# Kernel tuning notes

Measured on AMD Instinct MI355X. Metric: run time of the kernel, lower is better.

The kernel has to match this reference:

```python
import jax, jax.numpy as jnp
import numpy as np

D_MODEL = 512
N_HEADS = 8
D_K = D_MODEL // N_HEADS
WINDOW = 64
SCALE = 1.0 / np.sqrt(D_K)


def setup_inputs() -> dict:
    key = jax.random.key(0)
    ks = jax.random.split(key, 9)
    B, S = 1, 2048
    s = 1.0 / np.sqrt(D_MODEL)
    inp = {
        "x": jax.random.normal(ks[0], (B, S, D_MODEL), dtype=jnp.float32),
        "Wq": jax.random.normal(ks[1], (D_MODEL, D_MODEL), dtype=jnp.float32) * s,
        "bq": jnp.zeros((D_MODEL,), dtype=jnp.float32),
        "Wk": jax.random.normal(ks[2], (D_MODEL, D_MODEL), dtype=jnp.float32) * s,
        "bk": jnp.zeros((D_MODEL,), dtype=jnp.float32),
        "Wv": jax.random.normal(ks[3], (D_MODEL, D_MODEL), dtype=jnp.float32) * s,
        "bv": jnp.zeros((D_MODEL,), dtype=jnp.float32),
        "Wo": jax.random.normal(ks[4], (D_MODEL, D_MODEL), dtype=jnp.float32) * s,
        "bo": jnp.zeros((D_MODEL,), dtype=jnp.float32),
    }
    return inp


def reference(x, Wq, bq, Wk, bk, Wv, bv, Wo, bo):
    B, S, _ = x.shape
    # projections (torch Linear: x @ W.T + b); split heads -> [B,S,H,dk]
    q = (x @ Wq.T + bq).reshape(B, S, N_HEADS, D_K)
    k = (x @ Wk.T + bk).reshape(B, S, N_HEADS, D_K)
    v = (x @ Wv.T + bv).reshape(B, S, N_HEADS, D_K)

    # banded window indices: position i attends to [i-W, i+W]
    L = 2 * WINDOW + 1
    offsets = jnp.arange(L) - WINDOW                    # [L]
    pos = jnp.arange(S)[:, None] + offsets[None, :]     # [S, L]
    valid = (pos >= 0) & (pos < S)                      # [S, L]
    posc = jnp.clip(pos, 0, S - 1)

    k_w = k[:, posc]                                    # [B, S, L, H, dk]
    v_w = v[:, posc]                                    # [B, S, L, H, dk]

    scores = jnp.einsum("bshd,bslhd->bhsl", q, k_w) * SCALE
    scores = jnp.where(valid[None, None, :, :], scores, -jnp.inf)
    attn = jax.nn.softmax(scores, axis=-1)              # [B, H, S, L]
    out = jnp.einsum("bhsl,bslhd->bshd", attn, v_w)     # [B, S, H, dk]
    out = out.reshape(B, S, D_MODEL)
    return out @ Wo.T + bo
```

## Files before the change

### kernel.cpp

```cpp
#include <hip/hip_runtime.h>
#include <hip/hip_bf16.h>
#include <math.h>

#define S_LEN  2048
#define DMODEL 512
#define NHEADS 8
#define DK     64
#define WIN    64

static constexpr float SCALE = 0.125f;

typedef short bf16x8 __attribute__((ext_vector_type(8)));
typedef float f32x4  __attribute__((ext_vector_type(4)));

__device__ __forceinline__ short bfh(float v)
{
    __hip_bfloat16 b = __float2bfloat16(v);
    return *reinterpret_cast<short*>(&b);
}
__device__ __forceinline__ float bf2f(short s)
{
    __hip_bfloat16 b = *reinterpret_cast<__hip_bfloat16*>(&s);
    return __bfloat162float(b);
}
__device__ __forceinline__ void split1(float v, short& h, short& l)
{
    h = bfh(v);
    l = bfh(v - bf2f(h));
}

__device__ __forceinline__ void dma16(const void* g, void* l)
{
    __builtin_amdgcn_global_load_lds(
        (const __attribute__((address_space(1))) unsigned int*)g,
        (__attribute__((address_space(3))) unsigned int*)l, 16, 0, 0);
}

__global__ __launch_bounds__(256)
void prep(const float* __restrict__ x,
          const float* __restrict__ wq, const float* __restrict__ wk,
          const float* __restrict__ wv, const float* __restrict__ wo,
          short* __restrict__ xh, short* __restrict__ xl,
          short* __restrict__ wqb, short* __restrict__ wkb,
          short* __restrict__ wvb, short* __restrict__ wob)
{
    const int z = blockIdx.z;
    if (z == 0) {
        for (int i = blockIdx.x * 256 + threadIdx.x; i < 262144; i += gridDim.x * 256) {
            const float4 v = ((const float4*)x)[i];
            short4 h4, l4;
            split1(v.x, h4.x, l4.x);
            split1(v.y, h4.y, l4.y);
            split1(v.z, h4.z, l4.z);
            split1(v.w, h4.w, l4.w);
            ((short4*)xh)[i] = h4;
            ((short4*)xl)[i] = l4;
        }
    } else {
        const float* s; short* d;
        switch (z) {
            case 1:  s = wq; d = wqb; break;
            case 2:  s = wk; d = wkb; break;
            case 3:  s = wv; d = wvb; break;
            default: s = wo; d = wob; break;
        }
        for (int i = blockIdx.x * 256 + threadIdx.x; i < 65536; i += gridDim.x * 256) {
            const float4 v = ((const float4*)s)[i];
            short4 o;
            o.x = bfh(v.x); o.y = bfh(v.y); o.z = bfh(v.z); o.w = bfh(v.w);
            ((short4*)d)[i] = o;
        }
    }
}

__global__ __launch_bounds__(256)
void gemm_qkv8(const short* __restrict__ xh, const short* __restrict__ xl,
               const short* __restrict__ wqb, const short* __restrict__ wkb,
               const short* __restrict__ wvb,
               const float* __restrict__ bq, const float* __restrict__ bk,
               const float* __restrict__ bv,
               short* __restrict__ qb, short* __restrict__ kb,
               short* __restrict__ vbt)
{
    __shared__ __align__(16) short sW[64 * 512];

    const int z = blockIdx.z;
    const short* Bg   = (z == 0) ? wqb : (z == 1) ? wkb : wvb;
    const float* bias = (z == 0) ? bq  : (z == 1) ? bk  : bv;
    const int row0 = blockIdx.y * 64;
    const int col0 = blockIdx.x * 64;
    const int tid  = threadIdx.x;
    const int lane = tid & 63;
    const int wv   = tid >> 6;
    const int col  = lane & 15;
    const int quad = lane >> 4;
    const int m    = row0 + wv * 16 + col;

    for (int i = wv; i < 64; i += 4) {
        dma16(Bg + (size_t)(col0 + i) * 512 + (size_t)((lane ^ (i & 7)) * 8),
              sW + i * 512);
    }
    __syncthreads();

    f32x4 acc[4];
#pragma unroll
    for (int nj = 0; nj < 4; ++nj)
        acc[nj] = (f32x4)0.0f;

#pragma unroll 4
    for (int kc = 0; kc < 16; ++kc) {
        const size_t aoff = (size_t)m * 512 + kc * 32 + quad * 8;
        const bf16x8 ah = *(const bf16x8*)(xh + aoff);
        const bf16x8 al = *(const bf16x8*)(xl + aoff);
#pragma unroll
        for (int nj = 0; nj < 4; ++nj) {
            const int n = nj * 16 + col;
            const int c = kc * 4 + quad;
            const bf16x8 bf = *(const bf16x8*)&sW[n * 512 + ((c ^ (n & 7)) * 8)];
            acc[nj] = __builtin_amdgcn_mfma_f32_16x16x32_bf16(ah, bf, acc[nj], 0, 0, 0);
            acc[nj] = __builtin_amdgcn_mfma_f32_16x16x32_bf16(al, bf, acc[nj], 0, 0, 0);
        }
    }

#pragma unroll
    for (int nj = 0; nj < 4; ++nj) {
        const int cc = col0 + nj * 16 + col;
        const float bias_v = bias[cc];
#pragma unroll
        for (int e = 0; e < 4; ++e) {
            const int row = row0 + wv * 16 + quad * 4 + e;
            const float val = acc[nj][e] + bias_v;
            if (z == 0) {
                qb[(size_t)row * 512 + cc] = bfh(val);
            } else if (z == 1) {
                kb[(size_t)row * 512 + cc] = bfh(val);
            } else {
                vbt[(size_t)cc * 2048 + row] = bfh(val);
            }
        }
    }
}

__global__ __launch_bounds__(256)
void gemm_out8(const short* __restrict__ ah_g,
               const short* __restrict__ wob, const float* __restrict__ bo,
               float* __restrict__ out)
{
    __shared__ __align__(16) short sW[64 * 512];

    const int row0 = blockIdx.y * 64;
    const int col0 = blockIdx.x * 64;
    const int tid  = threadIdx.x;
    const int lane = tid & 63;
    const int wv   = tid >> 6;
    const int col  = lane & 15;
    const int quad = lane >> 4;
    const int m    = row0 + wv * 16 + col;

    for (int i = wv; i < 64; i += 4) {
        dma16(wob + (size_t)(col0 + i) * 512 + (size_t)((lane ^ (i & 7)) * 8),
              sW + i * 512);
    }
    __syncthreads();

    f32x4 acc[4];
#pragma unroll
    for (int nj = 0; nj < 4; ++nj)
        acc[nj] = (f32x4)0.0f;

#pragma unroll 4
    for (int kc = 0; kc < 16; ++kc) {
        const bf16x8 af = *(const bf16x8*)(ah_g + (size_t)m * 512 + kc * 32 + quad * 8);
#pragma unroll
        for (int nj = 0; nj < 4; ++nj) {
            const int n = nj * 16 + col;
            const int c = kc * 4 + quad;
            const bf16x8 bf = *(const bf16x8*)&sW[n * 512 + ((c ^ (n & 7)) * 8)];
            acc[nj] = __builtin_amdgcn_mfma_f32_16x16x32_bf16(af, bf, acc[nj], 0, 0, 0);
        }
    }

#pragma unroll
    for (int nj = 0; nj < 4; ++nj) {
        const int cc = col0 + nj * 16 + col;
        const float bias_v = bo[cc];
#pragma unroll
        for (int e = 0; e < 4; ++e) {
            const int row = row0 + wv * 16 + quad * 4 + e;
            out[(size_t)row * 512 + cc] = acc[nj][e] + bias_v;
        }
    }
}

__global__ __launch_bounds__(256)
void banded_attn6(const short* __restrict__ qb, const short* __restrict__ kb,
                  const short* __restrict__ vbt, short* __restrict__ abh)
{
    __shared__ __align__(16) short VtS[64 * 256];
    __shared__ __align__(16) short KS [192 * 64];
    __shared__ __align__(16) short QS [32 * 64];
    __shared__ float pmax[4][32];
    __shared__ float psum[4][32];
    short* PS = KS;

    const int h    = blockIdx.x;
    const int t0   = blockIdx.y * 32;
    const int tid  = threadIdx.x;
    const int lane = tid & 63;
    const int wv   = tid >> 6;
    const int col  = lane & 15;
    const int quad = lane >> 4;

    {
        const int lr = lane >> 3;
        const int lc = lane & 7;
        for (int i = wv; i < 28; i += 4) {
            const short* src; short* dst; int r;
            if (i < 4) {
                r = i * 8 + lr;
                src = qb + (size_t)(t0 + r) * 512 + h * 64;
                dst = QS + i * 512;
            } else {
                const int g = i - 4;
                r = g * 8 + lr;
                int pos = t0 - 64 + r;
                pos = pos < 0 ? 0 : (pos > 2047 ? 2047 : pos);
                src = kb + (size_t)pos * 512 + h * 64;
                dst = KS + g * 512;
            }
            const int cs = lc ^ (r & 7);
            dma16(src + cs * 8, dst);
        }
        for (int i = wv; i < 32; i += 4) {
            const int q = i * 64 + lane;
            const int d = q >> 5;
            const int b = q & 31;
            const int j0 = (b < 24) ? b : 0;
            const int j = j0 ^ (d & 7);
            int p0 = t0 - 64 + j * 8;
            p0 = p0 < 0 ? 0 : (p0 > 2040 ? 2040 : p0);
            dma16(vbt + (size_t)(h * 64 + d) * 2048 + p0, VtS + i * 512);
        }
    }
    __syncthreads();

    f32x4 sacc[2][3];
#pragma unroll
    for (int mi = 0; mi < 2; ++mi)
#pragma unroll
        for (int nj = 0; nj < 3; ++nj)
            sacc[mi][nj] = (f32x4)0.0f;

#pragma unroll
    for (int ks = 0; ks < 2; ++ks) {
        const int q0 = ks * 4 + quad;
        bf16x8 aq[2];
#pragma unroll
        for (int mi = 0; mi < 2; ++mi) {
            const int mm = mi * 16 + col;
            const int p = q0 ^ (mm & 7);
            aq[mi] = *(const bf16x8*)&QS[mm * 64 + p * 8];
        }
#pragma unroll
        for (int nj = 0; nj < 3; ++nj) {
            const int n = wv * 48 + nj * 16 + col;
            const int p = q0 ^ (n & 7);
            const bf16x8 bkf = *(const bf16x8*)&KS[n * 64 + p * 8];
#pragma unroll
            for (int mi = 0; mi < 2; ++mi)
                sacc[mi][nj] = __builtin_amdgcn_mfma_f32_16x16x32_bf16(aq[mi], bkf, sacc[mi][nj], 0, 0, 0);
        }
    }

    float pv[2][3][4];
#pragma unroll
    for (int mi = 0; mi < 2; ++mi)
#pragma unroll
        for (int nj = 0; nj < 3; ++nj)
#pragma unroll
            for (int e = 0; e < 4; ++e) {
                const int r32 = mi * 16 + quad * 4 + e;
                const int n   = wv * 48 + nj * 16 + col;
                const int pos = t0 - 64 + n;
                const int d   = n - r32;
                const bool valid = (pos >= 0) && (pos < S_LEN) && (d >= 0) && (d <= 128);
                pv[mi][nj][e] = valid ? sacc[mi][nj][e] * SCALE : -__builtin_inff();
            }

#pragma unroll
    for (int mi = 0; mi < 2; ++mi)
#pragma unroll
        for (int e = 0; e < 4; ++e) {
            float mx = fmaxf(fmaxf(pv[mi][0][e], pv[mi][1][e]), pv[mi][2][e]);
#pragma unroll
            for (int off = 1; off < 16; off <<= 1)
                mx = fmaxf(mx, __shfl_xor(mx, off));
            if ((lane & 15) == 0) pmax[wv][mi * 16 + quad * 4 + e] = mx;
        }
    __syncthreads();

#pragma unroll
    for (int mi = 0; mi < 2; ++mi)
#pragma unroll
        for (int e = 0; e < 4; ++e) {
            const int r32 = mi * 16 + quad * 4 + e;
            const float m = fmaxf(fmaxf(pmax[0][r32], pmax[1][r32]),
                                  fmaxf(pmax[2][r32], pmax[3][r32]));
            float ss = 0.f;
#pragma unroll
            for (int nj = 0; nj < 3; ++nj) {
                const float p = __expf(pv[mi][nj][e] - m);
                pv[mi][nj][e] = p;
                ss += p;
            }
#pragma unroll
            for (int off = 1; off < 16; off <<= 1)
                ss += __shfl_xor(ss, off);
            if ((lane & 15) == 0) psum[wv][r32] = ss;
#pragma unroll
            for (int nj = 0; nj < 3; ++nj) {
                const int n = wv * 48 + nj * 16 + col;
                PS[r32 * 200 + n] = bfh(pv[mi][nj][e]);
            }
        }
    __syncthreads();

    const int mi = wv >> 1;
    f32x4 oacc[2];
    oacc[0] = (f32x4)0.0f;
    oacc[1] = (f32x4)0.0f;
#pragma unroll
    for (int ks = 0; ks < 6; ++ks) {
        const bf16x8 pa = *(const bf16x8*)&PS[(mi * 16 + col) * 200 + ks * 32 + quad * 8];
#pragma unroll
        for (int t = 0; t < 2; ++t) {
            const int d = ((wv & 1) * 2 + t) * 16 + col;
            const int j = (ks * 4 + quad) ^ (d & 7);
            const bf16x8 vf = *(const bf16x8*)&VtS[d * 256 + j * 8];
            oacc[t] = __builtin_amdgcn_mfma_f32_16x16x32_bf16(pa, vf, oacc[t], 0, 0, 0);
        }
    }

    float linv[4];
#pragma unroll
    for (int e = 0; e < 4; ++e) {
        const int r32 = mi * 16 + quad * 4 + e;
        linv[e] = 1.0f / (psum[0][r32] + psum[1][r32] + psum[2][r32] + psum[3][r32]);
    }
#pragma unroll
    for (int t = 0; t < 2; ++t) {
        const int nj = (wv & 1) * 2 + t;
#pragma unroll
        for (int e = 0; e < 4; ++e) {
            const int r32 = mi * 16 + quad * 4 + e;
            const float val = oacc[t][e] * linv[e];
            const size_t idx = (size_t)(t0 + r32) * 512 + h * 64 + nj * 16 + col;
            abh[idx] = bfh(val);
        }
    }
}

extern "C" void kernel_launch(void* const* d_in, const int* in_sizes, int n_in,
                              void* d_out, int out_size, void* d_ws, size_t ws_size,
                              hipStream_t stream)
{
    const float* x  = (const float*)d_in[0];
    const float* Wq = (const float*)d_in[1];
    const float* bq = (const float*)d_in[2];
    const float* Wk = (const float*)d_in[3];
    const float* bk = (const float*)d_in[4];
    const float* Wv = (const float*)d_in[5];
    const float* bv = (const float*)d_in[6];
    const float* Wo = (const float*)d_in[7];
    const float* bo = (const float*)d_in[8];
    float* out = (float*)d_out;

    char* ws = (char*)d_ws;
    short* qb  = (short*)(ws);
    short* kb  = (short*)(ws + (2u << 20));
    short* vbt = (short*)(ws + (4u << 20));
    short* abh = (short*)(ws + (6u << 20));
    short* xh  = (short*)(ws + (8u << 20));
    short* xl  = (short*)(ws + (10u << 20));
    short* wqb = (short*)(ws + (12u << 20));
    short* wkb = (short*)(ws + (12u << 20) + 1 * (512u << 10));
    short* wvb = (short*)(ws + (12u << 20) + 2 * (512u << 10));
    short* wob = (short*)(ws + (12u << 20) + 3 * (512u << 10));

    dim3 gp(128, 1, 5);
    prep<<<gp, 256, 0, stream>>>(x, Wq, Wk, Wv, Wo,
                                 xh, xl, wqb, wkb, wvb, wob);

    dim3 gq(DMODEL / 64, S_LEN / 64, 3);
    gemm_qkv8<<<gq, 256, 0, stream>>>(xh, xl, wqb, wkb, wvb,
                                      bq, bk, bv, qb, kb, vbt);

    dim3 ga(NHEADS, S_LEN / 32);
    banded_attn6<<<ga, 256, 0, stream>>>(qb, kb, vbt, abh);

    dim3 go(DMODEL / 64, S_LEN / 64);
    gemm_out8<<<go, 256, 0, stream>>>(abh, wob, bo, out);
}
```

Before: 115.6 us.

## Fuse all stages into one cooperative persistent kernel with grid syncs

Replaces the four separate launches (prep, QKV GEMM, banded attention, output GEMM) with a single cooperative kernel of 512 blocks that runs each stage in turn, separated by grid-wide barriers. GEMM tiles shrink to 64x32 so every block does the same share of work, and each block loops over Q, K and V in sequence. The aim is to remove per-launch overhead and the gaps between kernels. In exchange it adds grid.sync costs, lowers per-stage parallelism because each block does serial work, and requires all 512 blocks to be resident at once, two per CU.

```diff
diff --git a/kernel.cpp b/kernel.cpp
--- a/kernel.cpp
+++ b/kernel.cpp
@@ -1,6 +1,9 @@
 #include <hip/hip_runtime.h>
+#include <hip/hip_cooperative_groups.h>
 #include <hip/hip_bf16.h>
 #include <math.h>
+
+namespace cg = cooperative_groups;
 
 #define S_LEN  2048
 #define DMODEL 512
@@ -36,326 +39,300 @@
         (__attribute__((address_space(3))) unsigned int*)l, 16, 0, 0);
 }
 
-__global__ __launch_bounds__(256)
-void prep(const float* __restrict__ x,
-          const float* __restrict__ wq, const float* __restrict__ wk,
-          const float* __restrict__ wv, const float* __restrict__ wo,
-          short* __restrict__ xh, short* __restrict__ xl,
-          short* __restrict__ wqb, short* __restrict__ wkb,
-          short* __restrict__ wvb, short* __restrict__ wob)
-{
-    const int z = blockIdx.z;
-    if (z == 0) {
-        for (int i = blockIdx.x * 256 + threadIdx.x; i < 262144; i += gridDim.x * 256) {
-            const float4 v = ((const float4*)x)[i];
+struct KParams {
+    const float *x, *Wq, *bq, *Wk, *bk, *Wv, *bv, *Wo, *bo;
+    float* out;
+    short *qb, *kb, *vbt, *abh, *xh, *xl, *wqb, *wkb, *wvb, *wob;
+};
+
+__global__ __launch_bounds__(256, 2)
+void fused(KParams p)
+{
+    __shared__ __align__(16) char smem[62464];
+    cg::grid_group grid = cg::this_grid();
+
+    const int bid  = blockIdx.x;
+    const int tid  = threadIdx.x;
+    const int lane = tid & 63;
+    const int wv   = tid >> 6;
+    const int col  = lane & 15;
+    const int quad = lane >> 4;
+
+    {
+        for (int i = bid * 256 + tid; i < 262144; i += 131072) {
+            const float4 v = ((const float4*)p.x)[i];
             short4 h4, l4;
             split1(v.x, h4.x, l4.x);
             split1(v.y, h4.y, l4.y);
             split1(v.z, h4.z, l4.z);
             split1(v.w, h4.w, l4.w);
-            ((short4*)xh)[i] = h4;
-            ((short4*)xl)[i] = l4;
-        }
-    } else {
-        const float* s; short* d;
-        switch (z) {
-            case 1:  s = wq; d = wqb; break;
-            case 2:  s = wk; d = wkb; break;
-            case 3:  s = wv; d = wvb; break;
-            default: s = wo; d = wob; break;
-        }
-        for (int i = blockIdx.x * 256 + threadIdx.x; i < 65536; i += gridDim.x * 256) {
+            ((short4*)p.xh)[i] = h4;
+            ((short4*)p.xl)[i] = l4;
+        }
+        for (int u = bid * 256 + tid; u < 262144; u += 131072) {
+            const int w = u >> 16;
+            const int i = u & 65535;
+            const float* s = (w == 0) ? p.Wq : (w == 1) ? p.Wk : (w == 2) ? p.Wv : p.Wo;
+            short*       d = (w == 0) ? p.wqb : (w == 1) ? p.wkb : (w == 2) ? p.wvb : p.wob;
             const float4 v = ((const float4*)s)[i];
             short4 o;
             o.x = bfh(v.x); o.y = bfh(v.y); o.z = bfh(v.z); o.w = bfh(v.w);
             ((short4*)d)[i] = o;
         }
     }
-}
-
-__global__ __launch_bounds__(256)
-void gemm_qkv8(const short* __restrict__ xh, const short* __restrict__ xl,
-               const short* __restrict__ wqb, const short* __restrict__ wkb,
-               const short* __restrict__ wvb,
-               const float* __restrict__ bq, const float* __restrict__ bk,
-               const float* __restrict__ bv,
-               short* __restrict__ qb, short* __restrict__ kb,
-               short* __restrict__ vbt)
-{
-    __shared__ __align__(16) short sW[64 * 512];
-
-    const int z = blockIdx.z;
-    const short* Bg   = (z == 0) ? wqb : (z == 1) ? wkb : wvb;
-    const float* bias = (z == 0) ? bq  : (z == 1) ? bk  : bv;
-    const int row0 = blockIdx.y * 64;
-    const int col0 = blockIdx.x * 64;
-    const int tid  = threadIdx.x;
-    const int lane = tid & 63;
-    const int wv   = tid >> 6;
-    const int col  = lane & 15;
-    const int quad = lane >> 4;
-    const int m    = row0 + wv * 16 + col;
-
-    for (int i = wv; i < 64; i += 4) {
-        dma16(Bg + (size_t)(col0 + i) * 512 + (size_t)((lane ^ (i & 7)) * 8),
-              sW + i * 512);
+    grid.sync();
+
+    {
+        short* sW = (short*)smem;
+        const int ct   = bid & 15;
+        const int rt   = bid >> 4;
+        const int col0 = ct * 32;
+        const int m    = rt * 64 + wv * 16 + col;
+
+        for (int z = 0; z < 3; ++z) {
+            const short* Bg   = (z == 0) ? p.wqb : (z == 1) ? p.wkb : p.wvb;
+            const float* bias = (z == 0) ? p.bq  : (z == 1) ? p.bk  : p.bv;
+
+            __syncthreads();
+            for (int i = wv; i < 32; i += 4)
+                dma16(Bg + (size_t)(col0 + i) * 512 + (size_t)((lane ^ (i & 7)) * 8),
+                      sW + i * 512);
+            __syncthreads();
+
+            f32x4 acc[2];
+            acc[0] = (f32x4)0.0f;
+            acc[1] = (f32x4)0.0f;
+
+#pragma unroll 4
+            for (int kc = 0; kc < 16; ++kc) {
+                const size_t aoff = (size_t)m * 512 + kc * 32 + quad * 8;
+                const bf16x8 ah = *(const bf16x8*)(p.xh + aoff);
+                const bf16x8 al = *(const bf16x8*)(p.xl + aoff);
+#pragma unroll
+                for (int nj = 0; nj < 2; ++nj) {
+                    const int n = nj * 16 + col;
+                    const int c = kc * 4 + quad;
+                    const bf16x8 bf = *(const bf16x8*)&sW[n * 512 + ((c ^ (n & 7)) * 8)];
+                    acc[nj] = __builtin_amdgcn_mfma_f32_16x16x32_bf16(ah, bf, acc[nj], 0, 0, 0);
+                    acc[nj] = __builtin_amdgcn_mfma_f32_16x16x32_bf16(al, bf, acc[nj], 0, 0, 0);
+                }
+            }
+
+#pragma unroll
+            for (int nj = 0; nj < 2; ++nj) {
+                const int cc = col0 + nj * 16 + col;
+                const float bias_v = bias[cc];
+#pragma unroll
+                for (int e = 0; e < 4; ++e) {
+                    const int row = rt * 64 + wv * 16 + quad * 4 + e;
+                    const float val = acc[nj][e] + bias_v;
+                    if (z == 0)      p.qb[(size_t)row * 512 + cc] = bfh(val);
+                    else if (z == 1) p.kb[(size_t)row * 512 + cc] = bfh(val);
+                    else             p.vbt[(size_t)cc * 2048 + row] = bfh(val);
+                }
+            }
+        }
     }
-    __syncthreads();
-
-    f32x4 acc[4];
-#pragma unroll
-    for (int nj = 0; nj < 4; ++nj)
-        acc[nj] = (f32x4)0.0f;
-
-#pragma unroll 4
-    for (int kc = 0; kc < 16; ++kc) {
-        const size_t aoff = (size_t)m * 512 + kc * 32 + quad * 8;
-        const bf16x8 ah = *(const bf16x8*)(xh + aoff);
-        const bf16x8 al = *(const bf16x8*)(xl + aoff);
-#pragma unroll
-        for (int nj = 0; nj < 4; ++nj) {
-            const int n = nj * 16 + col;
-            const int c = kc * 4 + quad;
-            const bf16x8 bf = *(const bf16x8*)&sW[n * 512 + ((c ^ (n & 7)) * 8)];
-            acc[nj] = __builtin_amdgcn_mfma_f32_16x16x32_bf16(ah, bf, acc[nj], 0, 0, 0);
-            acc[nj] = __builtin_amdgcn_mfma_f32_16x16x32_bf16(al, bf, acc[nj], 0, 0, 0);
-        }
-    }
-
-#pragma unroll
-    for (int nj = 0; nj < 4; ++nj) {
-        const int cc = col0 + nj * 16 + col;
-        const float bias_v = bias[cc];
-#pragma unroll
-        for (int e = 0; e < 4; ++e) {
-            const int row = row0 + wv * 16 + quad * 4 + e;
-            const float val = acc[nj][e] + bias_v;
-            if (z == 0) {
-                qb[(size_t)row * 512 + cc] = bfh(val);
-            } else if (z == 1) {
-                kb[(size_t)row * 512 + cc] = bfh(val);
-            } else {
-                vbt[(size_t)cc * 2048 + row] = bfh(val);
-            }
-        }
-    }
-}
-
-__global__ __launch_bounds__(256)
-void gemm_out8(const short* __restrict__ ah_g,
-               const short* __restrict__ wob, const float* __restrict__ bo,
-               float* __restrict__ out)
-{
-    __shared__ __align__(16) short sW[64 * 512];
-
-    const int row0 = blockIdx.y * 64;
-    const int col0 = blockIdx.x * 64;
-    const int tid  = threadIdx.x;
-    const int lane = tid & 63;
-    const int wv   = tid >> 6;
-    const int col  = lane & 15;
-    const int quad = lane >> 4;
-    const int m    = row0 + wv * 16 + col;
-
-    for (int i = wv; i < 64; i += 4) {
-        dma16(wob + (size_t)(col0 + i) * 512 + (size_t)((lane ^ (i & 7)) * 8),
-              sW + i * 512);
-    }
-    __syncthreads();
-
-    f32x4 acc[4];
-#pragma unroll
-    for (int nj = 0; nj < 4; ++nj)
-        acc[nj] = (f32x4)0.0f;
-
-#pragma unroll 4
-    for (int kc = 0; kc < 16; ++kc) {
-        const bf16x8 af = *(const bf16x8*)(ah_g + (size_t)m * 512 + kc * 32 + quad * 8);
-#pragma unroll
-        for (int nj = 0; nj < 4; ++nj) {
-            const int n = nj * 16 + col;
-            const int c = kc * 4 + quad;
-            const bf16x8 bf = *(const bf16x8*)&sW[n * 512 + ((c ^ (n & 7)) * 8)];
-            acc[nj] = __builtin_amdgcn_mfma_f32_16x16x32_bf16(af, bf, acc[nj], 0, 0, 0);
-        }
-    }
-
-#pragma unroll
-    for (int nj = 0; nj < 4; ++nj) {
-        const int cc = col0 + nj * 16 + col;
-        const float bias_v = bo[cc];
-#pragma unroll
-        for (int e = 0; e < 4; ++e) {
-            const int row = row0 + wv * 16 + quad * 4 + e;
-            out[(size_t)row * 512 + cc] = acc[nj][e] + bias_v;
-        }
-    }
-}
-
-__global__ __launch_bounds__(256)
-void banded_attn6(const short* __restrict__ qb, const short* __restrict__ kb,
-                  const short* __restrict__ vbt, short* __restrict__ abh)
-{
-    __shared__ __align__(16) short VtS[64 * 256];
-    __shared__ __align__(16) short KS [192 * 64];
-    __shared__ __align__(16) short QS [32 * 64];
-    __shared__ float pmax[4][32];
-    __shared__ float psum[4][32];
-    short* PS = KS;
-
-    const int h    = blockIdx.x;
-    const int t0   = blockIdx.y * 32;
-    const int tid  = threadIdx.x;
-    const int lane = tid & 63;
-    const int wv   = tid >> 6;
-    const int col  = lane & 15;
-    const int quad = lane >> 4;
+    grid.sync();
 
     {
-        const int lr = lane >> 3;
-        const int lc = lane & 7;
-        for (int i = wv; i < 28; i += 4) {
-            const short* src; short* dst; int r;
-            if (i < 4) {
-                r = i * 8 + lr;
-                src = qb + (size_t)(t0 + r) * 512 + h * 64;
-                dst = QS + i * 512;
-            } else {
-                const int g = i - 4;
-                r = g * 8 + lr;
-                int pos = t0 - 64 + r;
-                pos = pos < 0 ? 0 : (pos > 2047 ? 2047 : pos);
-                src = kb + (size_t)pos * 512 + h * 64;
-                dst = KS + g * 512;
-            }
-            const int cs = lc ^ (r & 7);
-            dma16(src + cs * 8, dst);
-        }
-        for (int i = wv; i < 32; i += 4) {
-            const int q = i * 64 + lane;
-            const int d = q >> 5;
-            const int b = q & 31;
-            const int j0 = (b < 24) ? b : 0;
-            const int j = j0 ^ (d & 7);
-            int p0 = t0 - 64 + j * 8;
-            p0 = p0 < 0 ? 0 : (p0 > 2040 ? 2040 : p0);
-            dma16(vbt + (size_t)(h * 64 + d) * 2048 + p0, VtS + i * 512);
-        }
-    }
-    __syncthreads();
-
-    f32x4 sacc[2][3];
-#pragma unroll
-    for (int mi = 0; mi < 2; ++mi)
-#pragma unroll
-        for (int nj = 0; nj < 3; ++nj)
-            sacc[mi][nj] = (f32x4)0.0f;
-
-#pragma unroll
-    for (int ks = 0; ks < 2; ++ks) {
-        const int q0 = ks * 4 + quad;
-        bf16x8 aq[2];
-#pragma unroll
-        for (int mi = 0; mi < 2; ++mi) {
-            const int mm = mi * 16 + col;
-            const int p = q0 ^ (mm & 7);
-            aq[mi] = *(const bf16x8*)&QS[mm * 64 + p * 8];
-        }
-#pragma unroll
-        for (int nj = 0; nj < 3; ++nj) {
-            const int n = wv * 48 + nj * 16 + col;
-            const int p = q0 ^ (n & 7);
-            const bf16x8 bkf = *(const bf16x8*)&KS[n * 64 + p * 8];
-#pragma unroll
-            for (int mi = 0; mi < 2; ++mi)
-                sacc[mi][nj] = __builtin_amdgcn_mfma_f32_16x16x32_bf16(aq[mi], bkf, sacc[mi][nj], 0, 0, 0);
-        }
-    }
-
-    float pv[2][3][4];
-#pragma unroll
-    for (int mi = 0; mi < 2; ++mi)
-#pragma unroll
-        for (int nj = 0; nj < 3; ++nj)
+        short* VtS = (short*)smem;
+        short* KS  = (short*)(smem + 32768);
+        short* QS  = (short*)(smem + 57344);
+        float (*pmax)[32] = (float(*)[32])(smem + 61440);
+        float (*psum)[32] = (float(*)[32])(smem + 61952);
+        short* PS = KS;
+
+        const int h  = bid >> 6;
+        const int t0 = (bid & 63) * 32;
+
+        {
+            const int lr = lane >> 3;
+            const int lc = lane & 7;
+            for (int i = wv; i < 28; i += 4) {
+                const short* src; short* dst; int r;
+                if (i < 4) {
+                    r = i * 8 + lr;
+                    src = p.qb + (size_t)(t0 + r) * 512 + h * 64;
+                    dst = QS + i * 512;
+                } else {
+                    const int g = i - 4;
+                    r = g * 8 + lr;
+                    int pos = t0 - 64 + r;
+                    pos = pos < 0 ? 0 : (pos > 2047 ? 2047 : pos);
+                    src = p.kb + (size_t)pos * 512 + h * 64;
+                    dst = KS + g * 512;
+                }
+                const int cs = lc ^ (r & 7);
+                dma16(src + cs * 8, dst);
+            }
+            for (int i = wv; i < 32; i += 4) {
+                const int q = i * 64 + lane;
+                const int d = q >> 5;
+                const int b = q & 31;
+                const int j0 = (b < 24) ? b : 0;
+                const int j = j0 ^ (d & 7);
+                int p0 = t0 - 64 + j * 8;
+                p0 = p0 < 0 ? 0 : (p0 > 2040 ? 2040 : p0);
+                dma16(p.vbt + (size_t)(h * 64 + d) * 2048 + p0, VtS + i * 512);
+            }
+        }
+        __syncthreads();
+
+        f32x4 sacc[2][3];
+#pragma unroll
+        for (int mi = 0; mi < 2; ++mi)
+#pragma unroll
+            for (int nj = 0; nj < 3; ++nj)
+                sacc[mi][nj] = (f32x4)0.0f;
+
+#pragma unroll
+        for (int ks = 0; ks < 2; ++ks) {
+            const int q0 = ks * 4 + quad;
+            bf16x8 aq[2];
+#pragma unroll
+            for (int mi = 0; mi < 2; ++mi) {
+                const int mm = mi * 16 + col;
+                const int pp = q0 ^ (mm & 7);
+                aq[mi] = *(const bf16x8*)&QS[mm * 64 + pp * 8];
+            }
+#pragma unroll
+            for (int nj = 0; nj < 3; ++nj) {
+                const int n = wv * 48 + nj * 16 + col;
+                const int pp = q0 ^ (n & 7);
+                const bf16x8 bkf = *(const bf16x8*)&KS[n * 64 + pp * 8];
+#pragma unroll
+                for (int mi = 0; mi < 2; ++mi)
+                    sacc[mi][nj] = __builtin_amdgcn_mfma_f32_16x16x32_bf16(aq[mi], bkf, sacc[mi][nj], 0, 0, 0);
+            }
+        }
+
+        float pv[2][3][4];
+#pragma unroll
+        for (int mi = 0; mi < 2; ++mi)
+#pragma unroll
+            for (int nj = 0; nj < 3; ++nj)
+#pragma unroll
+                for (int e = 0; e < 4; ++e) {
+                    const int r32 = mi * 16 + quad * 4 + e;
+                    const int n   = wv * 48 + nj * 16 + col;
+                    const int pos = t0 - 64 + n;
+                    const int d   = n - r32;
+                    const bool valid = (pos >= 0) && (pos < S_LEN) && (d >= 0) && (d <= 128);
+                    pv[mi][nj][e] = valid ? sacc[mi][nj][e] * SCALE : -__builtin_inff();
+                }
+
+#pragma unroll
+        for (int mi = 0; mi < 2; ++mi)
+#pragma unroll
+            for (int e = 0; e < 4; ++e) {
+                float mx = fmaxf(fmaxf(pv[mi][0][e], pv[mi][1][e]), pv[mi][2][e]);
+#pragma unroll
+                for (int off = 1; off < 16; off <<= 1)
+                    mx = fmaxf(mx, __shfl_xor(mx, off));
+                if ((lane & 15) == 0) pmax[wv][mi * 16 + quad * 4 + e] = mx;
+            }
+        __syncthreads();
+
+#pragma unroll
+        for (int mi = 0; mi < 2; ++mi)
 #pragma unroll
             for (int e = 0; e < 4; ++e) {
                 const int r32 = mi * 16 + quad * 4 + e;
-                const int n   = wv * 48 + nj * 16 + col;
-                const int pos = t0 - 64 + n;
-                const int d   = n - r32;
-                const bool valid = (pos >= 0) && (pos < S_LEN) && (d >= 0) && (d <= 128);
-                pv[mi][nj][e] = valid ? sacc[mi][nj][e] * SCALE : -__builtin_inff();
-            }
-
-#pragma unroll
-    for (int mi = 0; mi < 2; ++mi)
-#pragma unroll
-        for (int e = 0; e < 4; ++e) {
-            float mx = fmaxf(fmaxf(pv[mi][0][e], pv[mi][1][e]), pv[mi][2][e]);
-#pragma unroll
-            for (int off = 1; off < 16; off <<= 1)
-                mx = fmaxf(mx, __shfl_xor(mx, off));
-            if ((lane & 15) == 0) pmax[wv][mi * 16 + quad * 4 + e] = mx;
-        }
-    __syncthreads();
-
-#pragma unroll
-    for (int mi = 0; mi < 2; ++mi)
+                const float m = fmaxf(fmaxf(pmax[0][r32], pmax[1][r32]),
+                                      fmaxf(pmax[2][r32], pmax[3][r32]));
+                float ss = 0.f;
+#pragma unroll
+                for (int nj = 0; nj < 3; ++nj) {
+                    const float pe = __expf(pv[mi][nj][e] - m);
+                    pv[mi][nj][e] = pe;
+                    ss += pe;
+                }
+#pragma unroll
+                for (int off = 1; off < 16; off <<= 1)
+                    ss += __shfl_xor(ss, off);
+                if ((lane & 15) == 0) psum[wv][r32] = ss;
+#pragma unroll
+                for (int nj = 0; nj < 3; ++nj) {
+                    const int n = wv * 48 + nj * 16 + col;
+                    PS[r32 * 200 + n] = bfh(pv[mi][nj][e]);
+                }
+            }
+        __syncthreads();
+
+        const int mi = wv >> 1;
+        f32x4 oacc[2];
+        oacc[0] = (f32x4)0.0f;
+        oacc[1] = (f32x4)0.0f;
+#pragma unroll
+        for (int ks = 0; ks < 6; ++ks) {
+            const bf16x8 pa = *(const bf16x8*)&PS[(mi * 16 + col) * 200 + ks * 32 + quad * 8];
+#pragma unroll
+            for (int t = 0; t < 2; ++t) {
+                const int d = ((wv & 1) * 2 + t) * 16 + col;
+                const int j = (ks * 4 + quad) ^ (d & 7);
+                const bf16x8 vf = *(const bf16x8*)&VtS[d * 256 + j * 8];
+                oacc[t] = __builtin_amdgcn_mfma_f32_16x16x32_bf16(pa, vf, oacc[t], 0, 0, 0);
+            }
+        }
+
+        float linv[4];
 #pragma unroll
         for (int e = 0; e < 4; ++e) {
             const int r32 = mi * 16 + quad * 4 + e;
-            const float m = fmaxf(fmaxf(pmax[0][r32], pmax[1][r32]),
-                                  fmaxf(pmax[2][r32], pmax[3][r32]));
-            float ss = 0.f;
-#pragma unroll
-            for (int nj = 0; nj < 3; ++nj) {
-                const float p = __expf(pv[mi][nj][e] - m);
-                pv[mi][nj][e] = p;
-                ss += p;
-            }
-#pragma unroll
-            for (int off = 1; off < 16; off <<= 1)
-                ss += __shfl_xor(ss, off);
-            if ((lane & 15) == 0) psum[wv][r32] = ss;
-#pragma unroll
-            for (int nj = 0; nj < 3; ++nj) {
-                const int n = wv * 48 + nj * 16 + col;
-                PS[r32 * 200 + n] = bfh(pv[mi][nj][e]);
-            }
-        }
-    __syncthreads();
-
-    const int mi = wv >> 1;
-    f32x4 oacc[2];
-    oacc[0] = (f32x4)0.0f;
-    oacc[1] = (f32x4)0.0f;
-#pragma unroll
-    for (int ks = 0; ks < 6; ++ks) {
-        const bf16x8 pa = *(const bf16x8*)&PS[(mi * 16 + col) * 200 + ks * 32 + quad * 8];
+            linv[e] = 1.0f / (psum[0][r32] + psum[1][r32] + psum[2][r32] + psum[3][r32]);
+        }
 #pragma unroll
         for (int t = 0; t < 2; ++t) {
-            const int d = ((wv & 1) * 2 + t) * 16 + col;
-            const int j = (ks * 4 + quad) ^ (d & 7);
-            const bf16x8 vf = *(const bf16x8*)&VtS[d * 256 + j * 8];
-            oacc[t] = __builtin_amdgcn_mfma_f32_16x16x32_bf16(pa, vf, oacc[t], 0, 0, 0);
+            const int nj = (wv & 1) * 2 + t;
+#pragma unroll
+            for (int e = 0; e < 4; ++e) {
+                const int r32 = mi * 16 + quad * 4 + e;
+                const float val = oacc[t][e] * linv[e];
+                const size_t idx = (size_t)(t0 + r32) * 512 + h * 64 + nj * 16 + col;
+                p.abh[idx] = bfh(val);
+            }
         }
     }
-
-    float linv[4];
-#pragma unroll
-    for (int e = 0; e < 4; ++e) {
-        const int r32 = mi * 16 + quad * 4 + e;
-        linv[e] = 1.0f / (psum[0][r32] + psum[1][r32] + psum[2][r32] + psum[3][r32]);
-    }
-#pragma unroll
-    for (int t = 0; t < 2; ++t) {
-        const int nj = (wv & 1) * 2 + t;
-#pragma unroll
-        for (int e = 0; e < 4; ++e) {
-            const int r32 = mi * 16 + quad * 4 + e;
-            const float val = oacc[t][e] * linv[e];
-            const size_t idx = (size_t)(t0 + r32) * 512 + h * 64 + nj * 16 + col;
-            abh[idx] = bfh(val);
+    grid.sync();
+
+    {
+        short* sW = (short*)smem;
+        const int ct   = bid & 15;
+        const int rt   = bid >> 4;
+        const int col0 = ct * 32;
+        const int m    = rt * 64 + wv * 16 + col;
+
+        for (int i = wv; i < 32; i += 4)
+            dma16(p.wob + (size_t)(col0 + i) * 512 + (size_t)((lane ^ (i & 7)) * 8),
+                  sW + i * 512);
+        __syncthreads();
+
+        f32x4 acc[2];
+        acc[0] = (f32x4)0.0f;
+        acc[1] = (f32x4)0.0f;
+
+#pragma unroll 4
+        for (int kc = 0; kc < 16; ++kc) {
+            const bf16x8 af = *(const bf16x8*)(p.abh + (size_t)m * 512 + kc * 32 + quad * 8);
+#pragma unroll
+            for (int nj = 0; nj < 2; ++nj) {
+                const int n = nj * 16 + col;
+                const int c = kc * 4 + quad;
+                const bf16x8 bf = *(const bf16x8*)&sW[n * 512 + ((c ^ (n & 7)) * 8)];
+                acc[nj] = __builtin_amdgcn_mfma_f32_16x16x32_bf16(af, bf, acc[nj], 0, 0, 0);
+            }
+        }
+
+#pragma unroll
+        for (int nj = 0; nj < 2; ++nj) {
+            const int cc = col0 + nj * 16 + col;
+            const float bias_v = p.bo[cc];
+#pragma unroll
+            for (int e = 0; e < 4; ++e) {
+                const int row = rt * 64 + wv * 16 + quad * 4 + e;
+                p.out[(size_t)row * 512 + cc] = acc[nj][e] + bias_v;
+            }
         }
     }
 }
@@ -364,40 +341,30 @@
                               void* d_out, int out_size, void* d_ws, size_t ws_size,
                               hipStream_t stream)
 {
-    const float* x  = (const float*)d_in[0];
-    const float* Wq = (const float*)d_in[1];
-    const float* bq = (const float*)d_in[2];
-    const float* Wk = (const float*)d_in[3];
-    const float* bk = (const float*)d_in[4];
-    const float* Wv = (const float*)d_in[5];
-    const float* bv = (const float*)d_in[6];
-    const float* Wo = (const float*)d_in[7];
-    const float* bo = (const float*)d_in[8];
-    float* out = (float*)d_out;
-
     char* ws = (char*)d_ws;
-    short* qb  = (short*)(ws);
-    short* kb  = (short*)(ws + (2u << 20));
-    short* vbt = (short*)(ws + (4u << 20));
-    short* abh = (short*)(ws + (6u << 20));
-    short* xh  = (short*)(ws + (8u << 20));
-    short* xl  = (short*)(ws + (10u << 20));
-    short* wqb = (short*)(ws + (12u << 20));
-    short* wkb = (short*)(ws + (12u << 20) + 1 * (512u << 10));
-    short* wvb = (short*)(ws + (12u << 20) + 2 * (512u << 10));
-    short* wob = (short*)(ws + (12u << 20) + 3 * (512u << 10));
-
-    dim3 gp(128, 1, 5);
-    prep<<<gp, 256, 0, stream>>>(x, Wq, Wk, Wv, Wo,
-                                 xh, xl, wqb, wkb, wvb, wob);
-
-    dim3 gq(DMODEL / 64, S_LEN / 64, 3);
-    gemm_qkv8<<<gq, 256, 0, stream>>>(xh, xl, wqb, wkb, wvb,
-                                      bq, bk, bv, qb, kb, vbt);
-
-    dim3 ga(NHEADS, S_LEN / 32);
-    banded_attn6<<<ga, 256, 0, stream>>>(qb, kb, vbt, abh);
-
-    dim3 go(DMODEL / 64, S_LEN / 64);
-    gemm_out8<<<go, 256, 0, stream>>>(abh, wob, bo, out);
-}
+    KParams p;
+    p.x  = (const float*)d_in[0];
+    p.Wq = (const float*)d_in[1];
+    p.bq = (const float*)d_in[2];
+    p.Wk = (const float*)d_in[3];
+    p.bk = (const float*)d_in[4];
+    p.Wv = (const float*)d_in[5];
+    p.bv = (const float*)d_in[6];
+    p.Wo = (const float*)d_in[7];
+    p.bo = (const float*)d_in[8];
+    p.out = (float*)d_out;
+    p.qb  = (short*)(ws);
+    p.kb  = (short*)(ws + (2u << 20));
+    p.vbt = (short*)(ws + (4u << 20));
+    p.abh = (short*)(ws + (6u << 20));
+    p.xh  = (short*)(ws + (8u << 20));
+    p.xl  = (short*)(ws + (10u << 20));
+    p.wqb = (short*)(ws + (12u << 20));
+    p.wkb = (short*)(ws + (12u << 20) + 1 * (512u << 10));
+    p.wvb = (short*)(ws + (12u << 20) + 2 * (512u << 10));
+    p.wob = (short*)(ws + (12u << 20) + 3 * (512u << 10));
+
+    void* args[] = { &p };
+    hipLaunchCooperativeKernel((const void*)fused, dim3(512), dim3(256),
+                               args, 0, stream);
+}
```

New measurement: 313.6 us. 2.71x slower.
